# Optimization experiments

Hardware: AMD Instinct MI355X
Metric: run time of the kernel (lower is better)

Reference implementation:

```python
import jax, jax.numpy as jnp
import numpy as np
from jax.scipy.special import digamma, gammaln

COEF = 0.01
PRIOR = 1.0
IGNORE_INDEX = 255


def setup_inputs() -> dict:
    key = jax.random.key(0)
    k1, k2 = jax.random.split(key)
    pred = jax.random.normal(k1, (8, 19, 512, 512), dtype=jnp.float32)
    target = jax.random.randint(k2, (8, 512, 512), 0, 19, dtype=jnp.int64)
    return {"pred": pred, "target": target}


def reference(pred, target):
    # pred: [B, C, H, W] logits; target: [B, H, W] int class ids
    alphas = jnp.exp(pred)
    mask_ignore = target == IGNORE_INDEX
    tgt = jnp.where(mask_ignore, 0, target)
    # gather alpha at the answer class: [B, H, W]
    a_ans = jnp.take_along_axis(alphas, tgt[:, None, :, :], axis=1)[:, 0]
    a_zero = jnp.sum(alphas, axis=1)  # [B, H, W]
    ll_loss = digamma(a_ans) - digamma(a_zero)
    loss1 = gammaln(a_zero) - jnp.sum(gammaln(alphas), axis=1)
    loss2 = jnp.sum((alphas - PRIOR) * (digamma(alphas) - digamma(a_zero)[:, None, :, :]), axis=1)
    kl_loss = loss1 + loss2
    loss = COEF * kl_loss - ll_loss  # [B, H, W]
    loss = jnp.where(mask_ignore, jnp.zeros_like(loss), loss)
    avg_factor = jnp.sum(target != IGNORE_INDEX).astype(loss.dtype)
    return jnp.sum(loss) / avg_factor
```

## Files before the change

### kernel.cpp

```cpp
#include <hip/hip_runtime.h>


#define NCLS 19
#define HW (512 * 512)
#define NPIX (8 * HW)
#define IGNORE_IDX 255

#define PC1 0.08333333333f
#define PC2 0.00833333333f
#define PC3 0.00396825397f
#define GL1 0.08333333333f
#define GL2 0.00277777778f
#define GL3 0.00079365079f
#define HLN2PI 0.918938533205f
#define LN2F 0.693147180560f

__device__ __forceinline__ float fast_rcp(float x) { return __builtin_amdgcn_rcpf(x); }

struct Acc {
    float a0, s2, slgy, dgans;
    double ppd;
};

__device__ __forceinline__ void chan(float x, int c, int tc, Acc& A) {
    float a  = __expf(x);
    float a1 = a + 1.f, a2 = a + 2.f, y = a + 3.f;
    float p  = a * a1 * a2;
    float rpy = fast_rcp(p * y);
    float r  = p * rpy;
    float rp = y * rpy;
    float q  = __fmaf_rn(a, __fmaf_rn(a, 3.f, 6.f), 2.f);
    float ly = __logf(y);
    float r2 = r * r;
    float psiy = ly - 0.5f * r - r2 * (PC1 - r2 * (PC2 - r2 * PC3));
    float psia = psiy - q * rp;
    A.s2 = __fmaf_rn(a - 1.f, psia, A.s2);
    A.a0 += a;
    float lgy = __fmaf_rn(y - 0.5f, ly, -y) + HLN2PI
                + r * (GL1 - r2 * (GL2 - r2 * GL3));
    A.slgy += lgy;
    A.ppd *= (double)p;
    A.dgans = (c == tc) ? psia : A.dgans;
}

__device__ __forceinline__ float finish(const Acc& A) {
    float a0 = A.a0;
    float a1 = a0 + 1.f, a2 = a0 + 2.f, y = a0 + 3.f;
    float p  = a0 * a1 * a2;
    float rpy = fast_rcp(p * y);
    float r  = p * rpy, rp = y * rpy;
    float q  = __fmaf_rn(a0, __fmaf_rn(a0, 3.f, 6.f), 2.f);
    float ly = __logf(y);
    float r2 = r * r;
    float psi0 = ly - 0.5f * r - r2 * (PC1 - r2 * (PC2 - r2 * PC3)) - q * rp;
    float lg0  = __fmaf_rn(y - 0.5f, ly, -y) + HLN2PI
                 + r * (GL1 - r2 * (GL2 - r2 * GL3)) - __logf(p);
    int hi = __double2hiint(A.ppd);
    int lo = __double2loint(A.ppd);
    int e  = ((hi >> 20) & 0x7FF) - 1023;
    double mant = __hiloint2double((hi & 0x000FFFFF) | 0x3FF00000, lo);
    float lnpp = __logf((float)mant) + (float)e * LN2F;

    float ll    = A.dgans - psi0;
    float loss1 = lg0 - (A.slgy - lnpp);
    float loss2 = A.s2 - psi0 * (a0 - (float)NCLS);
    return 0.01f * (loss1 + loss2) - ll;
}

__global__ __launch_bounds__(256) void bml_main(const float* __restrict__ pred,
                                                const int* __restrict__ target,
                                                double* __restrict__ ws) {
    int g  = blockIdx.x * blockDim.x + threadIdx.x;
    int p4 = g << 2;
    int b  = p4 >> 18;
    int hw = p4 & (HW - 1);
    const float4* base = (const float4*)(pred + (size_t)b * NCLS * HW + hw);

    int4 t4 = *(const int4*)(target + p4);
    int tc0 = (t4.x == IGNORE_IDX) ? 0 : t4.x;
    int tc1 = (t4.y == IGNORE_IDX) ? 0 : t4.y;
    int tc2 = (t4.z == IGNORE_IDX) ? 0 : t4.z;
    int tc3 = (t4.w == IGNORE_IDX) ? 0 : t4.w;

    Acc A0 = {0.f, 0.f, 0.f, 0.f, 1.0};
    Acc A1 = {0.f, 0.f, 0.f, 0.f, 1.0};
    Acc A2 = {0.f, 0.f, 0.f, 0.f, 1.0};
    Acc A3 = {0.f, 0.f, 0.f, 0.f, 1.0};

    #pragma unroll 2
    for (int c = 0; c < NCLS; ++c) {
        float4 x = base[(size_t)c * (HW / 4)];
        chan(x.x, c, tc0, A0);
        chan(x.y, c, tc1, A1);
        chan(x.z, c, tc2, A2);
        chan(x.w, c, tc3, A3);
    }

    float l0 = finish(A0), l1 = finish(A1), l2 = finish(A2), l3 = finish(A3);

    float local = 0.f;
    unsigned cnt = 0;
    if (t4.x != IGNORE_IDX) { local += l0; cnt++; }
    if (t4.y != IGNORE_IDX) { local += l1; cnt++; }
    if (t4.z != IGNORE_IDX) { local += l2; cnt++; }
    if (t4.w != IGNORE_IDX) { local += l3; cnt++; }

    #pragma unroll
    for (int off = 32; off; off >>= 1) {
        local += __shfl_down(local, off);
        cnt   += __shfl_down(cnt, off);
    }
    __shared__ float s_sum[4];
    __shared__ unsigned s_cnt[4];
    int lane = threadIdx.x & 63, wid = threadIdx.x >> 6;
    if (lane == 0) { s_sum[wid] = local; s_cnt[wid] = cnt; }
    __syncthreads();
    if (threadIdx.x == 0) {
        float bs = s_sum[0] + s_sum[1] + s_sum[2] + s_sum[3];
        unsigned bc = s_cnt[0] + s_cnt[1] + s_cnt[2] + s_cnt[3];
        atomicAdd(&ws[0], (double)bs);
        atomicAdd(&ws[1], (double)bc);
    }
}

__global__ void bml_finalize(const double* __restrict__ ws, float* __restrict__ out) {
    if (threadIdx.x == 0 && blockIdx.x == 0)
        out[0] = (float)(ws[0] / ws[1]);
}

extern "C" void kernel_launch(void* const* d_in, const int* in_sizes, int n_in,
                              void* d_out, int out_size, void* d_ws, size_t ws_size,
                              hipStream_t stream) {
    const float* pred = (const float*)d_in[0];
    const int* target = (const int*)d_in[1];
    float* out = (float*)d_out;
    double* ws = (double*)d_ws;

    hipMemsetAsync(d_ws, 0, 2 * sizeof(double), stream);

    const int block = 256;
    const int grid = NPIX / (block * 4);
    bml_main<<<grid, block, 0, stream>>>(pred, target, ws);
    bml_finalize<<<1, 64, 0, stream>>>(ws, out);
}
```

Measured before the change: 263.0 us.

## Use 2 pixels per thread, prefetch all channels, shorten digamma/lgamma shift

Each thread now handles two pixels instead of four and issues all 19 channel loads up front into registers before computing, which raises memory-level parallelism and doubles the grid. The asymptotic digamma/lgamma series now starts from a+2 instead of a+3 and drops one term, with FMA-form evaluation, which cuts per-channel ALU work. The shorter shift and truncated series lower accuracy for small alphas. Holding all loads in registers raises register pressure.

New measurement: 277.4 us. +5.5%, slower.

```diff
diff --git a/kernel.cpp b/kernel.cpp
--- a/kernel.cpp
+++ b/kernel.cpp
@@ -8,10 +8,8 @@
 
 #define PC1 0.08333333333f
 #define PC2 0.00833333333f
-#define PC3 0.00396825397f
 #define GL1 0.08333333333f
 #define GL2 0.00277777778f
-#define GL3 0.00079365079f
 #define HLN2PI 0.918938533205f
 #define LN2F 0.693147180560f
 
@@ -24,20 +22,20 @@
 
 __device__ __forceinline__ void chan(float x, int c, int tc, Acc& A) {
     float a  = __expf(x);
-    float a1 = a + 1.f, a2 = a + 2.f, y = a + 3.f;
-    float p  = a * a1 * a2;
+    float a1 = a + 1.f, y = a + 2.f;
+    float p  = a * a1;
     float rpy = fast_rcp(p * y);
     float r  = p * rpy;
     float rp = y * rpy;
-    float q  = __fmaf_rn(a, __fmaf_rn(a, 3.f, 6.f), 2.f);
+    float q  = __fmaf_rn(2.f, a, 1.f);
     float ly = __logf(y);
     float r2 = r * r;
-    float psiy = ly - 0.5f * r - r2 * (PC1 - r2 * (PC2 - r2 * PC3));
-    float psia = psiy - q * rp;
+    float psiy = __fmaf_rn(-r2, __fmaf_rn(-r2, PC2, PC1), __fmaf_rn(-0.5f, r, ly));
+    float psia = __fmaf_rn(-q, rp, psiy);
     A.s2 = __fmaf_rn(a - 1.f, psia, A.s2);
     A.a0 += a;
     float lgy = __fmaf_rn(y - 0.5f, ly, -y) + HLN2PI
-                + r * (GL1 - r2 * (GL2 - r2 * GL3));
+                + r * __fmaf_rn(-r2, GL2, GL1);
     A.slgy += lgy;
     A.ppd *= (double)p;
     A.dgans = (c == tc) ? psia : A.dgans;
@@ -45,16 +43,17 @@
 
 __device__ __forceinline__ float finish(const Acc& A) {
     float a0 = A.a0;
-    float a1 = a0 + 1.f, a2 = a0 + 2.f, y = a0 + 3.f;
-    float p  = a0 * a1 * a2;
+    float a1 = a0 + 1.f, y = a0 + 2.f;
+    float p  = a0 * a1;
     float rpy = fast_rcp(p * y);
     float r  = p * rpy, rp = y * rpy;
-    float q  = __fmaf_rn(a0, __fmaf_rn(a0, 3.f, 6.f), 2.f);
+    float q  = __fmaf_rn(2.f, a0, 1.f);
     float ly = __logf(y);
     float r2 = r * r;
-    float psi0 = ly - 0.5f * r - r2 * (PC1 - r2 * (PC2 - r2 * PC3)) - q * rp;
+    float psi0 = __fmaf_rn(-r2, __fmaf_rn(-r2, PC2, PC1), __fmaf_rn(-0.5f, r, ly))
+                 - q * rp;
     float lg0  = __fmaf_rn(y - 0.5f, ly, -y) + HLN2PI
-                 + r * (GL1 - r2 * (GL2 - r2 * GL3)) - __logf(p);
+                 + r * __fmaf_rn(-r2, GL2, GL1) - __logf(p);
     int hi = __double2hiint(A.ppd);
     int lo = __double2loint(A.ppd);
     int e  = ((hi >> 20) & 0x7FF) - 1023;
@@ -70,40 +69,35 @@
 __global__ __launch_bounds__(256) void bml_main(const float* __restrict__ pred,
                                                 const int* __restrict__ target,
                                                 double* __restrict__ ws) {
-    int g  = blockIdx.x * blockDim.x + threadIdx.x;
-    int p4 = g << 2;
-    int b  = p4 >> 18;
-    int hw = p4 & (HW - 1);
-    const float4* base = (const float4*)(pred + (size_t)b * NCLS * HW + hw);
+    int tid = blockIdx.x * blockDim.x + threadIdx.x;
+    int p2  = tid << 1;
+    int b   = p2 >> 18;
+    int hw  = p2 & (HW - 1);
+    const float2* base = (const float2*)(pred + (size_t)b * NCLS * HW + hw);
 
-    int4 t4 = *(const int4*)(target + p4);
-    int tc0 = (t4.x == IGNORE_IDX) ? 0 : t4.x;
-    int tc1 = (t4.y == IGNORE_IDX) ? 0 : t4.y;
-    int tc2 = (t4.z == IGNORE_IDX) ? 0 : t4.z;
-    int tc3 = (t4.w == IGNORE_IDX) ? 0 : t4.w;
+    int2 t2 = *(const int2*)(target + p2);
+    int tc0 = (t2.x == IGNORE_IDX) ? 0 : t2.x;
+    int tc1 = (t2.y == IGNORE_IDX) ? 0 : t2.y;
+
+    float2 xs[NCLS];
+    #pragma unroll
+    for (int c = 0; c < NCLS; ++c)
+        xs[c] = base[c * (HW / 2)];
 
     Acc A0 = {0.f, 0.f, 0.f, 0.f, 1.0};
     Acc A1 = {0.f, 0.f, 0.f, 0.f, 1.0};
-    Acc A2 = {0.f, 0.f, 0.f, 0.f, 1.0};
-    Acc A3 = {0.f, 0.f, 0.f, 0.f, 1.0};
-
-    #pragma unroll 2
+    #pragma unroll
     for (int c = 0; c < NCLS; ++c) {
-        float4 x = base[(size_t)c * (HW / 4)];
-        chan(x.x, c, tc0, A0);
-        chan(x.y, c, tc1, A1);
-        chan(x.z, c, tc2, A2);
-        chan(x.w, c, tc3, A3);
+        chan(xs[c].x, c, tc0, A0);
+        chan(xs[c].y, c, tc1, A1);
     }
 
-    float l0 = finish(A0), l1 = finish(A1), l2 = finish(A2), l3 = finish(A3);
+    float l0 = finish(A0), l1 = finish(A1);
 
     float local = 0.f;
     unsigned cnt = 0;
-    if (t4.x != IGNORE_IDX) { local += l0; cnt++; }
-    if (t4.y != IGNORE_IDX) { local += l1; cnt++; }
-    if (t4.z != IGNORE_IDX) { local += l2; cnt++; }
-    if (t4.w != IGNORE_IDX) { local += l3; cnt++; }
+    if (t2.x != IGNORE_IDX) { local += l0; cnt++; }
+    if (t2.y != IGNORE_IDX) { local += l1; cnt++; }
 
     #pragma unroll
     for (int off = 32; off; off >>= 1) {
@@ -139,7 +133,7 @@
     hipMemsetAsync(d_ws, 0, 2 * sizeof(double), stream);
 
     const int block = 256;
-    const int grid = NPIX / (block * 4);
+    const int grid = NPIX / (block * 2);
     bml_main<<<grid, block, 0, stream>>>(pred, target, ws);
     bml_finalize<<<1, 64, 0, stream>>>(ws, out);
 }
```

## Shift digamma/lgamma by one step and preload all channels before compute

Applied to the files above, without the earlier changes.

The series for digamma and lgamma is now evaluated at a+1 with a single recurrence step instead of a+3 with three. The double-precision product used for the log-gamma correction is replaced by summing the raw logits, since log(exp(x)) = x. All 19 channel loads are issued up front into registers behind a scheduling barrier, and launch bounds request two blocks per CU. This cuts per-element ALU work and double-precision math and exposes more memory-level parallelism, but the asymptotic series is less accurate at small arguments and register pressure rises.

After: 244.3 us. 7.1% less time.

```diff
diff --git a/kernel.cpp b/kernel.cpp
--- a/kernel.cpp
+++ b/kernel.cpp
@@ -12,68 +12,63 @@
 #define GL1 0.08333333333f
 #define GL2 0.00277777778f
 #define GL3 0.00079365079f
-#define HLN2PI 0.918938533205f
-#define LN2F 0.693147180560f
+#define HLN2PI 0.9189385332f
+#define SUM_HLN2PI 17.45983213f
 
 __device__ __forceinline__ float fast_rcp(float x) { return __builtin_amdgcn_rcpf(x); }
 
 struct Acc {
-    float a0, s2, slgy, dgans;
-    double ppd;
+    float a0, s2, slgy, sx, dgans;
 };
 
 __device__ __forceinline__ void chan(float x, int c, int tc, Acc& A) {
-    float a  = __expf(x);
-    float a1 = a + 1.f, a2 = a + 2.f, y = a + 3.f;
-    float p  = a * a1 * a2;
-    float rpy = fast_rcp(p * y);
-    float r  = p * rpy;
-    float rp = y * rpy;
-    float q  = __fmaf_rn(a, __fmaf_rn(a, 3.f, 6.f), 2.f);
-    float ly = __logf(y);
-    float r2 = r * r;
-    float psiy = ly - 0.5f * r - r2 * (PC1 - r2 * (PC2 - r2 * PC3));
-    float psia = psiy - q * rp;
+    float a   = __expf(x);
+    float y   = a + 1.f;
+    float rpy = fast_rcp(a * y);
+    float r   = a * rpy;
+    float rp  = y * rpy;
+    float ly  = __logf(y);
+    float r2  = r * r;
+    float T   = __fmaf_rn(-r2, __fmaf_rn(-r2, PC3, PC2), PC1);
+    float psiy = __fmaf_rn(-r2, T, __fmaf_rn(-0.5f, r, ly));
+    float psia = psiy - rp;
     A.s2 = __fmaf_rn(a - 1.f, psia, A.s2);
     A.a0 += a;
-    float lgy = __fmaf_rn(y - 0.5f, ly, -y) + HLN2PI
-                + r * (GL1 - r2 * (GL2 - r2 * GL3));
-    A.slgy += lgy;
-    A.ppd *= (double)p;
+    float G   = __fmaf_rn(-r2, __fmaf_rn(-r2, GL3, GL2), GL1);
+    float lgp = __fmaf_rn(y - 0.5f, ly, -y);
+    A.slgy = __fmaf_rn(r, G, A.slgy + lgp);
+    A.sx += x;
     A.dgans = (c == tc) ? psia : A.dgans;
 }
 
 __device__ __forceinline__ float finish(const Acc& A) {
-    float a0 = A.a0;
-    float a1 = a0 + 1.f, a2 = a0 + 2.f, y = a0 + 3.f;
-    float p  = a0 * a1 * a2;
-    float rpy = fast_rcp(p * y);
-    float r  = p * rpy, rp = y * rpy;
-    float q  = __fmaf_rn(a0, __fmaf_rn(a0, 3.f, 6.f), 2.f);
-    float ly = __logf(y);
-    float r2 = r * r;
-    float psi0 = ly - 0.5f * r - r2 * (PC1 - r2 * (PC2 - r2 * PC3)) - q * rp;
-    float lg0  = __fmaf_rn(y - 0.5f, ly, -y) + HLN2PI
-                 + r * (GL1 - r2 * (GL2 - r2 * GL3)) - __logf(p);
-    int hi = __double2hiint(A.ppd);
-    int lo = __double2loint(A.ppd);
-    int e  = ((hi >> 20) & 0x7FF) - 1023;
-    double mant = __hiloint2double((hi & 0x000FFFFF) | 0x3FF00000, lo);
-    float lnpp = __logf((float)mant) + (float)e * LN2F;
+    float a0  = A.a0;
+    float y   = a0 + 1.f;
+    float rpy = fast_rcp(a0 * y);
+    float r   = a0 * rpy;
+    float rp  = y * rpy;
+    float ly  = __logf(y);
+    float la  = __logf(a0);
+    float r2  = r * r;
+    float T   = __fmaf_rn(-r2, __fmaf_rn(-r2, PC3, PC2), PC1);
+    float psi0 = __fmaf_rn(-r2, T, __fmaf_rn(-0.5f, r, ly)) - rp;
+    float G   = __fmaf_rn(-r2, __fmaf_rn(-r2, GL3, GL2), GL1);
+    float lg0 = __fmaf_rn(y - 0.5f, ly, -y) + HLN2PI + r * G - la;
 
+    float sum_lg = A.slgy + SUM_HLN2PI - A.sx;
     float ll    = A.dgans - psi0;
-    float loss1 = lg0 - (A.slgy - lnpp);
+    float loss1 = lg0 - sum_lg;
     float loss2 = A.s2 - psi0 * (a0 - (float)NCLS);
     return 0.01f * (loss1 + loss2) - ll;
 }
 
-__global__ __launch_bounds__(256) void bml_main(const float* __restrict__ pred,
-                                                const int* __restrict__ target,
-                                                double* __restrict__ ws) {
-    int g  = blockIdx.x * blockDim.x + threadIdx.x;
-    int p4 = g << 2;
-    int b  = p4 >> 18;
-    int hw = p4 & (HW - 1);
+__global__ __launch_bounds__(256, 2) void bml_main(const float* __restrict__ pred,
+                                                   const int* __restrict__ target,
+                                                   double* __restrict__ ws) {
+    int tid = blockIdx.x * blockDim.x + threadIdx.x;
+    int p4  = tid << 2;
+    int b   = p4 >> 18;
+    int hw  = p4 & (HW - 1);
     const float4* base = (const float4*)(pred + (size_t)b * NCLS * HW + hw);
 
     int4 t4 = *(const int4*)(target + p4);
@@ -82,18 +77,22 @@
     int tc2 = (t4.z == IGNORE_IDX) ? 0 : t4.z;
     int tc3 = (t4.w == IGNORE_IDX) ? 0 : t4.w;
 
-    Acc A0 = {0.f, 0.f, 0.f, 0.f, 1.0};
-    Acc A1 = {0.f, 0.f, 0.f, 0.f, 1.0};
-    Acc A2 = {0.f, 0.f, 0.f, 0.f, 1.0};
-    Acc A3 = {0.f, 0.f, 0.f, 0.f, 1.0};
+    float4 xs[NCLS];
+    #pragma unroll
+    for (int c = 0; c < NCLS; ++c)
+        xs[c] = base[c * (HW / 4)];
+    __builtin_amdgcn_sched_barrier(0);
 
-    #pragma unroll 2
+    Acc A0 = {0.f, 0.f, 0.f, 0.f, 0.f};
+    Acc A1 = {0.f, 0.f, 0.f, 0.f, 0.f};
+    Acc A2 = {0.f, 0.f, 0.f, 0.f, 0.f};
+    Acc A3 = {0.f, 0.f, 0.f, 0.f, 0.f};
+    #pragma unroll
     for (int c = 0; c < NCLS; ++c) {
-        float4 x = base[(size_t)c * (HW / 4)];
-        chan(x.x, c, tc0, A0);
-        chan(x.y, c, tc1, A1);
-        chan(x.z, c, tc2, A2);
-        chan(x.w, c, tc3, A3);
+        chan(xs[c].x, c, tc0, A0);
+        chan(xs[c].y, c, tc1, A1);
+        chan(xs[c].z, c, tc2, A2);
+        chan(xs[c].w, c, tc3, A3);
     }
 
     float l0 = finish(A0), l1 = finish(A1), l2 = finish(A2), l3 = finish(A3);
```
